# Kernel optimization log

Hardware: AMD Instinct MI355X
Metric: run time of the kernel (lower is better)

Reference implementation:

```python
import jax, jax.numpy as jnp
import numpy as np

N = 100000       # nodes
E = 1600000      # edges
V = 50000        # vocab
H = 256          # embedding dim (hsize)
A = 64           # per-head out dim (asize)
NH = 3           # num_heads
G = 64           # graphs in batch


def setup_inputs() -> dict:
    key = jax.random.key(0)
    ks = jax.random.split(key, 12)
    h0 = jax.random.randint(ks[0], (N,), 0, V)
    src = jax.random.randint(ks[1], (E,), 0, N)
    dst = jax.random.randint(ks[2], (E,), 0, N)
    graph_ids = jnp.sort(jax.random.randint(ks[3], (N,), 0, G))
    s = 0.05
    emb = jax.random.normal(ks[4], (V, H), jnp.float32) * s
    W_fc = jax.random.normal(ks[5], (H, NH * A), jnp.float32) * s   # GATConv fc
    attn_l = jax.random.normal(ks[6], (NH, A), jnp.float32) * s
    attn_r = jax.random.normal(ks[7], (NH, A), jnp.float32) * s
    bias_gat = jax.random.normal(ks[8], (NH, A), jnp.float32) * s
    W1 = jax.random.normal(ks[9], (A, 128), jnp.float32) * s
    b1 = jnp.zeros((128,), jnp.float32)
    W2 = jax.random.normal(ks[10], (128, 16), jnp.float32) * s
    b2 = jnp.zeros((16,), jnp.float32)
    return dict(h0=h0, src=src, dst=dst, graph_ids=graph_ids, emb=emb,
                W_fc=W_fc, attn_l=attn_l, attn_r=attn_r, bias_gat=bias_gat,
                W1=W1, b1=b1, W2=W2, b2=b2)


def reference(h0, src, dst, graph_ids, emb, W_fc, attn_l, attn_r, bias_gat,
              W1, b1, W2, b2):
    # embedding lookup
    h1 = emb[h0]                                            # [N, H]
    # GATConv: linear projection per head
    feat = (h1 @ W_fc).reshape(N, NH, A)                    # [N, NH, A]
    el = jnp.einsum('nha,ha->nh', feat, attn_l)             # [N, NH]
    er = jnp.einsum('nha,ha->nh', feat, attn_r)             # [N, NH]
    e = jax.nn.leaky_relu(el[src] + er[dst], 0.2)           # [E, NH]
    # segment softmax over incoming edges of each dst node
    m = jax.ops.segment_max(e, dst, num_segments=N)         # [N, NH]
    e_exp = jnp.exp(e - m[dst])                             # [E, NH]
    denom = jax.ops.segment_sum(e_exp, dst, num_segments=N) # [N, NH]
    alpha = e_exp / denom[dst]                              # [E, NH]
    # scatter-aggregate messages
    msg = alpha[:, :, None] * feat[src]                     # [E, NH, A]
    rst = jax.ops.segment_sum(msg, dst, num_segments=N)     # [N, NH, A]
    rst = rst + bias_gat[None]                              # GATConv bias
    # relu + mean over heads
    h2 = jnp.mean(jax.nn.relu(rst), axis=1)                 # [N, A]
    # MLP predictor: ReLU then Identity
    h3 = jax.nn.relu(h2 @ W1 + b1) @ W2 + b2                # [N, 16]
    # dgl.mean_nodes: per-graph mean readout
    sums = jax.ops.segment_sum(h3, graph_ids, num_segments=G)            # [G, 16]
    counts = jax.ops.segment_sum(jnp.ones((N,), h3.dtype), graph_ids, num_segments=G)
    return sums / jnp.maximum(counts, 1.0)[:, None]         # [G, 16]
```

## Files before the change

### kernel.cpp

```cpp
#include <hip/hip_runtime.h>
#include <hip/hip_bf16.h>

#define NNODES 100000
#define NEDGES 1600000
#define VOCAB 50000
#define HDIM 256
#define ADIM 64
#define NHEADS 3
#define FDIM 192
#define NGRAPH 64
#define NPART 64

typedef __attribute__((ext_vector_type(8))) short bf16x8;
typedef __attribute__((ext_vector_type(4))) float f32x4;

__device__ __forceinline__ float bf2f(unsigned short u) {
  return __uint_as_float((unsigned int)u << 16);
}
__device__ __forceinline__ unsigned short f2bf(float f) {
  unsigned int u = __float_as_uint(f);
  u += 0x7FFFu + ((u >> 16) & 1u);
  return (unsigned short)(u >> 16);
}

__global__ __launch_bounds__(256) void conv_emb_kernel(
    const float* __restrict__ emb, unsigned short* __restrict__ emb_bf, int n)
{
  int i = (blockIdx.x * 256 + threadIdx.x) * 4;
  if (i >= n) return;
  float4 v = *reinterpret_cast<const float4*>(&emb[i]);
  ushort4 o;
  o.x = f2bf(v.x); o.y = f2bf(v.y); o.z = f2bf(v.z); o.w = f2bf(v.w);
  *reinterpret_cast<ushort4*>(&emb_bf[i]) = o;
}

__global__ __launch_bounds__(256) void conv_weights_kernel(
    const float* __restrict__ Wfc, const float* __restrict__ W1,
    const float* __restrict__ W2, unsigned short* __restrict__ Wt,
    unsigned short* __restrict__ W1t, unsigned short* __restrict__ W2t)
{
  int i = blockIdx.x * 256 + threadIdx.x;
  if (i < HDIM * FDIM) {
    int c = i / HDIM, k = i % HDIM;
    Wt[i] = f2bf(Wfc[(size_t)k * FDIM + c]);
  } else if (i < HDIM * FDIM + 128 * 64) {
    int j = i - HDIM * FDIM;
    int c = j / 64, k = j % 64;
    W1t[j] = f2bf(W1[(size_t)k * 128 + c]);
  } else if (i < HDIM * FDIM + 128 * 64 + 16 * 128) {
    int j = i - HDIM * FDIM - 128 * 64;
    int c = j / 128, k = j % 128;
    W2t[j] = f2bf(W2[(size_t)k * 16 + c]);
  }
}

__global__ __launch_bounds__(256) void proj_gemm_kernel(
    const unsigned short* __restrict__ emb_bf,
    const unsigned short* __restrict__ Wt,
    unsigned short* __restrict__ proj_bf,
    int V)
{
  const int wave = threadIdx.x >> 6;
  const int lane = threadIdx.x & 63;
  const int row0 = blockIdx.x * 64 + wave * 16;
  int arow = row0 + (lane & 15);
  if (arow >= V) arow = V - 1;
  const int kgrp = (lane >> 4) * 8;

  f32x4 acc[12];
#pragma unroll
  for (int c = 0; c < 12; ++c) acc[c] = (f32x4){0.f, 0.f, 0.f, 0.f};

  const unsigned short* arow_p = &emb_bf[(size_t)arow * HDIM + kgrp];
  const unsigned short* bcol_p = &Wt[(size_t)(lane & 15) * HDIM + kgrp];

#pragma unroll
  for (int ks = 0; ks < 8; ++ks) {
    bf16x8 a = *reinterpret_cast<const bf16x8*>(arow_p + ks * 32);
#pragma unroll
    for (int c = 0; c < 12; ++c) {
      bf16x8 b = *reinterpret_cast<const bf16x8*>(bcol_p + (size_t)c * 16 * HDIM + ks * 32);
      acc[c] = __builtin_amdgcn_mfma_f32_16x16x32_bf16(a, b, acc[c], 0, 0, 0);
    }
  }
  const int cb = lane & 15;
  const int rb = row0 + 4 * (lane >> 4);
#pragma unroll
  for (int i = 0; i < 4; ++i) {
    int r = rb + i;
    if (r < V) {
#pragma unroll
      for (int c = 0; c < 12; ++c)
        proj_bf[(size_t)r * FDIM + c * 16 + cb] = f2bf(acc[c][i]);
    }
  }
}

__global__ __launch_bounds__(256) void vattn_kernel(
    const unsigned short* __restrict__ proj_bf, const float* __restrict__ attn_l,
    const float* __restrict__ attn_r, float* __restrict__ elv,
    float* __restrict__ erv, int V)
{
  int v    = blockIdx.x * 4 + (threadIdx.x >> 6);
  int lane = threadIdx.x & 63;
  if (v >= V) return;
  float sl[3], sr[3];
#pragma unroll
  for (int h = 0; h < 3; ++h) {
    float f = bf2f(proj_bf[(size_t)v * FDIM + h * 64 + lane]);
    sl[h] = f * attn_l[h * 64 + lane];
    sr[h] = f * attn_r[h * 64 + lane];
  }
#pragma unroll
  for (int s = 32; s > 0; s >>= 1) {
#pragma unroll
    for (int h = 0; h < 3; ++h) {
      sl[h] += __shfl_xor(sl[h], s, 64);
      sr[h] += __shfl_xor(sr[h], s, 64);
    }
  }
  if (lane == 0) {
#pragma unroll
    for (int h = 0; h < 3; ++h) { elv[v * 3 + h] = sl[h]; erv[v * 3 + h] = sr[h]; }
  }
}

__global__ __launch_bounds__(256) void ngather_kernel(
    const int* __restrict__ h0, const float* __restrict__ elv,
    const float* __restrict__ erv, float* __restrict__ nel,
    float* __restrict__ ner, int N)
{
  int n = blockIdx.x * 256 + threadIdx.x;
  if (n >= N) return;
  int v = h0[n];
#pragma unroll
  for (int h = 0; h < 3; ++h) {
    nel[n * 3 + h] = elv[v * 3 + h];
    ner[n * 3 + h] = erv[v * 3 + h];
  }
}

__global__ __launch_bounds__(256) void hist_kernel(
    const int* __restrict__ dst, int* __restrict__ cnt, int E)
{
  int e = blockIdx.x * 256 + threadIdx.x;
  if (e < E) atomicAdd(&cnt[dst[e]], 1);
}

__global__ __launch_bounds__(256) void scan_sum_kernel(
    const int* __restrict__ cnt, int* __restrict__ bsum, int n)
{
  __shared__ int red[256];
  int t = threadIdx.x;
  int base = blockIdx.x * 1024 + t * 4;
  int s = 0;
#pragma unroll
  for (int j = 0; j < 4; ++j) if (base + j < n) s += cnt[base + j];
  red[t] = s;
  __syncthreads();
  for (int o = 128; o > 0; o >>= 1) {
    if (t < o) red[t] += red[t + o];
    __syncthreads();
  }
  if (t == 0) bsum[blockIdx.x] = red[0];
}

__global__ void scan_bsum_kernel(int* bsum, int nb)
{
  if (threadIdx.x == 0 && blockIdx.x == 0) {
    int acc = 0;
    for (int i = 0; i < nb; ++i) { int v = bsum[i]; bsum[i] = acc; acc += v; }
  }
}

__global__ __launch_bounds__(256) void scan_write_kernel(
    const int* __restrict__ cnt, const int* __restrict__ bsum,
    int* __restrict__ offs, int n, int total)
{
  __shared__ int sd[256];
  int t = threadIdx.x;
  int base = blockIdx.x * 1024 + t * 4;
  int c[4];
  int ts = 0;
#pragma unroll
  for (int j = 0; j < 4; ++j) { c[j] = (base + j < n) ? cnt[base + j] : 0; ts += c[j]; }
  sd[t] = ts;
  __syncthreads();
  for (int o = 1; o < 256; o <<= 1) {
    int v = (t >= o) ? sd[t - o] : 0;
    __syncthreads();
    sd[t] += v;
    __syncthreads();
  }
  int run = sd[t] - ts + bsum[blockIdx.x];
#pragma unroll
  for (int j = 0; j < 4; ++j) {
    if (base + j < n) offs[base + j] = run;
    run += c[j];
  }
  if (blockIdx.x == 0 && t == 0) offs[n] = total;
}

__global__ __launch_bounds__(256) void scatter_kernel(
    const int* __restrict__ src, const int* __restrict__ dst,
    const int* __restrict__ h0,
    const float* __restrict__ nel, const float* __restrict__ ner,
    const int* __restrict__ offs, int* __restrict__ cursor,
    uint2* __restrict__ recs, int E)
{
  int e = blockIdx.x * 256 + threadIdx.x;
  if (e >= E) return;
  int s = src[e], d = dst[e];
  float w[3];
#pragma unroll
  for (int h = 0; h < 3; ++h) {
    float ev = nel[s * 3 + h] + ner[d * 3 + h];
    ev = ev > 0.f ? ev : 0.2f * ev;
    w[h] = __expf(ev);
  }
  int p = offs[d] + atomicAdd(&cursor[d], 1);
  uint2 r;
  r.x = (unsigned)h0[s] | ((unsigned)f2bf(w[0]) << 16);
  r.y = (unsigned)f2bf(w[1]) | ((unsigned)f2bf(w[2]) << 16);
  recs[p] = r;
}

__global__ __launch_bounds__(256) void aggregate_kernel(
    const uint2* __restrict__ recs, const int* __restrict__ offs,
    const unsigned short* __restrict__ proj_bf, const float* __restrict__ bias_gat,
    unsigned short* __restrict__ h2bf, int N)
{
  int lane = threadIdx.x & 63;
  int n = blockIdx.x * 4 + (threadIdx.x >> 6);
  if (n >= N) return;
  int lo = offs[n], hi = offs[n + 1];
  float a0 = 0.f, a1 = 0.f, a2 = 0.f, d0 = 0.f, d1 = 0.f, d2 = 0.f;

  int i = lo;
  for (; i + 4 <= hi; i += 4) {
    uint2 r[4];
#pragma unroll
    for (int j = 0; j < 4; ++j) r[j] = recs[i + j];
    const unsigned short* ps[4];
#pragma unroll
    for (int j = 0; j < 4; ++j)
      ps[j] = &proj_bf[(size_t)(r[j].x & 0xFFFFu) * FDIM];
    float g0[4], g1[4], g2[4];
#pragma unroll
    for (int j = 0; j < 4; ++j) {
      g0[j] = bf2f(ps[j][lane]);
      g1[j] = bf2f(ps[j][64 + lane]);
      g2[j] = bf2f(ps[j][128 + lane]);
    }
#pragma unroll
    for (int j = 0; j < 4; ++j) {
      float w0 = bf2f((unsigned short)(r[j].x >> 16));
      float w1 = bf2f((unsigned short)(r[j].y & 0xFFFFu));
      float w2 = bf2f((unsigned short)(r[j].y >> 16));
      a0 += w0 * g0[j]; a1 += w1 * g1[j]; a2 += w2 * g2[j];
      d0 += w0; d1 += w1; d2 += w2;
    }
  }
  for (; i < hi; ++i) {
    uint2 r = recs[i];
    const unsigned short* ps = &proj_bf[(size_t)(r.x & 0xFFFFu) * FDIM];
    float w0 = bf2f((unsigned short)(r.x >> 16));
    float w1 = bf2f((unsigned short)(r.y & 0xFFFFu));
    float w2 = bf2f((unsigned short)(r.y >> 16));
    a0 += w0 * bf2f(ps[lane]);
    a1 += w1 * bf2f(ps[64 + lane]);
    a2 += w2 * bf2f(ps[128 + lane]);
    d0 += w0; d1 += w1; d2 += w2;
  }

  float i0 = d0 > 0.f ? 1.f / d0 : 0.f;
  float i1 = d1 > 0.f ? 1.f / d1 : 0.f;
  float i2 = d2 > 0.f ? 1.f / d2 : 0.f;
  float r0 = a0 * i0 + bias_gat[lane];
  float r1 = a1 * i1 + bias_gat[64 + lane];
  float r2 = a2 * i2 + bias_gat[128 + lane];
  float h2 = (fmaxf(r0, 0.f) + fmaxf(r1, 0.f) + fmaxf(r2, 0.f)) * (1.f / 3.f);
  h2bf[(size_t)n * 64 + lane] = f2bf(h2);
}

__global__ __launch_bounds__(256) void post_mfma_kernel(
    const unsigned short* __restrict__ h2bf,
    const unsigned short* __restrict__ W1t,
    const float* __restrict__ b1,
    const unsigned short* __restrict__ W2t,
    const float* __restrict__ b2, const int* __restrict__ gid,
    float* __restrict__ sums_priv, float* __restrict__ counts_priv, int N)
{
  __shared__ unsigned short z_lds[64 * 128];
  const int wave = threadIdx.x >> 6;
  const int lane = threadIdx.x & 63;
  const int r = lane & 15;
  const int q = lane >> 4;
  const int kg = q * 8;
  const int rw0 = blockIdx.x * 64 + wave * 16;

  int arow = rw0 + r;
  if (arow >= N) arow = N - 1;

  f32x4 acc1[8];
#pragma unroll
  for (int c = 0; c < 8; ++c) acc1[c] = (f32x4){0.f, 0.f, 0.f, 0.f};

#pragma unroll
  for (int ks = 0; ks < 2; ++ks) {
    bf16x8 a = *reinterpret_cast<const bf16x8*>(&h2bf[(size_t)arow * 64 + kg + ks * 32]);
#pragma unroll
    for (int c = 0; c < 8; ++c) {
      bf16x8 b = *reinterpret_cast<const bf16x8*>(&W1t[(size_t)(c * 16 + r) * 64 + kg + ks * 32]);
      acc1[c] = __builtin_amdgcn_mfma_f32_16x16x32_bf16(a, b, acc1[c], 0, 0, 0);
    }
  }
#pragma unroll
  for (int c = 0; c < 8; ++c) {
    float bb = b1[c * 16 + r];
#pragma unroll
    for (int i = 0; i < 4; ++i) {
      float z = acc1[c][i] + bb;
      z = z > 0.f ? z : 0.f;
      z_lds[(wave * 16 + 4 * q + i) * 128 + c * 16 + r] = f2bf(z);
    }
  }
  __syncthreads();

  f32x4 acc2 = (f32x4){0.f, 0.f, 0.f, 0.f};
#pragma unroll
  for (int ks = 0; ks < 4; ++ks) {
    bf16x8 a = *reinterpret_cast<const bf16x8*>(&z_lds[(wave * 16 + r) * 128 + kg + ks * 32]);
    bf16x8 b = *reinterpret_cast<const bf16x8*>(&W2t[(size_t)r * 128 + kg + ks * 32]);
    acc2 = __builtin_amdgcn_mfma_f32_16x16x32_bf16(a, b, acc2, 0, 0, 0);
  }
  const int part = blockIdx.x & (NPART - 1);
  float bb2 = b2[r];
#pragma unroll
  for (int i = 0; i < 4; ++i) {
    int row = rw0 + 4 * q + i;
    if (row < N) {
      int g = gid[row];
      atomicAdd(&sums_priv[(part * NGRAPH + g) * 16 + r], acc2[i] + bb2);
      if (r == 0) atomicAdd(&counts_priv[part * NGRAPH + g], 1.f);
    }
  }
}

__global__ void finalize_kernel(const float* __restrict__ sums_priv,
                                const float* __restrict__ counts_priv,
                                float* __restrict__ out)
{
  int j = threadIdx.x;
  int g = j >> 4;
  float s = 0.f, c = 0.f;
  for (int p = 0; p < NPART; ++p) {
    s += sums_priv[p * NGRAPH * 16 + j];
    c += counts_priv[p * NGRAPH + g];
  }
  out[j] = s / fmaxf(c, 1.f);
}

extern "C" void kernel_launch(void* const* d_in, const int* in_sizes, int n_in,
                              void* d_out, int out_size, void* d_ws, size_t ws_size,
                              hipStream_t stream)
{
  const int*   h0  = (const int*)  d_in[0];
  const int*   src = (const int*)  d_in[1];
  const int*   dst = (const int*)  d_in[2];
  const int*   gid = (const int*)  d_in[3];
  const float* emb = (const float*)d_in[4];
  const float* Wfc = (const float*)d_in[5];
  const float* al  = (const float*)d_in[6];
  const float* ar  = (const float*)d_in[7];
  const float* bg  = (const float*)d_in[8];
  const float* W1  = (const float*)d_in[9];
  const float* b1  = (const float*)d_in[10];
  const float* W2  = (const float*)d_in[11];
  const float* b2  = (const float*)d_in[12];
  float* out = (float*)d_out;

  char* ws = (char*)d_ws;
  size_t off = 0;
  auto alloc = [&](size_t bytes) -> void* {
    off = (off + 255) & ~(size_t)255;
    void* p = ws + off;
    off += bytes;
    return p;
  };
  unsigned short* emb_bf  = (unsigned short*)alloc((size_t)VOCAB * HDIM * 2);
  unsigned short* Wt      = (unsigned short*)alloc((size_t)FDIM * HDIM * 2);
  unsigned short* W1t     = (unsigned short*)alloc((size_t)128 * 64 * 2);
  unsigned short* W2t     = (unsigned short*)alloc((size_t)16 * 128 * 2);
  unsigned short* proj_bf = (unsigned short*)alloc((size_t)VOCAB * FDIM * 2);
  unsigned short* h2bf    = (unsigned short*)alloc((size_t)NNODES * 64 * 2);
  uint2*  recs   = (uint2*) alloc((size_t)NEDGES * 8);
  float*  elv    = (float*) alloc((size_t)VOCAB * 3 * 4);
  float*  erv    = (float*) alloc((size_t)VOCAB * 3 * 4);
  float*  nel    = (float*) alloc((size_t)NNODES * 3 * 4);
  float*  ner    = (float*) alloc((size_t)NNODES * 3 * 4);
  int*    cnt    = (int*)   alloc((size_t)NNODES * 4);
  int*    offs   = (int*)   alloc((size_t)(NNODES + 1) * 4);
  int*    cursor = (int*)   alloc((size_t)NNODES * 4);
  int*    bsum   = (int*)   alloc((size_t)128 * 4);
  float*  sums   = (float*) alloc((size_t)NPART * NGRAPH * 16 * 4);
  float*  cnts   = (float*) alloc((size_t)NPART * NGRAPH * 4);

  hipMemsetAsync(cnt,    0, (size_t)NNODES * 4, stream);
  hipMemsetAsync(cursor, 0, (size_t)NNODES * 4, stream);
  hipMemsetAsync(sums,   0, (size_t)NPART * NGRAPH * 16 * 4, stream);
  hipMemsetAsync(cnts,   0, (size_t)NPART * NGRAPH * 4, stream);

  const int NB = (NNODES + 1023) / 1024;

  conv_emb_kernel<<<(VOCAB * HDIM / 4 + 255) / 256, 256, 0, stream>>>(
      emb, emb_bf, VOCAB * HDIM);
  conv_weights_kernel<<<(HDIM * FDIM + 128 * 64 + 16 * 128 + 255) / 256, 256, 0, stream>>>(
      Wfc, W1, W2, Wt, W1t, W2t);
  proj_gemm_kernel<<<(VOCAB + 63) / 64, 256, 0, stream>>>(emb_bf, Wt, proj_bf, VOCAB);
  vattn_kernel<<<(VOCAB + 3) / 4, 256, 0, stream>>>(proj_bf, al, ar, elv, erv, VOCAB);
  ngather_kernel<<<(NNODES + 255) / 256, 256, 0, stream>>>(h0, elv, erv, nel, ner, NNODES);
  hist_kernel<<<(NEDGES + 255) / 256, 256, 0, stream>>>(dst, cnt, NEDGES);
  scan_sum_kernel<<<NB, 256, 0, stream>>>(cnt, bsum, NNODES);
  scan_bsum_kernel<<<1, 64, 0, stream>>>(bsum, NB);
  scan_write_kernel<<<NB, 256, 0, stream>>>(cnt, bsum, offs, NNODES, NEDGES);
  scatter_kernel<<<(NEDGES + 255) / 256, 256, 0, stream>>>(src, dst, h0, nel, ner, offs,
                                                           cursor, recs, NEDGES);
  aggregate_kernel<<<(NNODES + 3) / 4, 256, 0, stream>>>(recs, offs, proj_bf, bg,
                                                         h2bf, NNODES);
  post_mfma_kernel<<<(NNODES + 63) / 64, 256, 0, stream>>>(h2bf, W1t, b1, W2t, b2, gid,
                                                           sums, cnts, NNODES);
  finalize_kernel<<<1, 1024, 0, stream>>>(sums, cnts, out);
}
```

Before: 393.2 us.

## Fuse emb conversion and attention scores into projection GEMM, shrink edge records

Folds the fp32-to-bf16 embedding conversion and the per-vocab attention dot products into the projection GEMM epilogue, removing the conv_emb, vattn and ngather kernels. The histogram kernel now records each edge's atomic rank, so scatter needs no second atomic cursor pass. Edge records shrink from 8-byte packed weights to a 16-bit vocab index, and attention weights are recomputed in the aggregate kernel from float4 el/er tables. This cuts launches and edge-array traffic but adds exp work and an extra gather per edge during aggregation. It also assumes per-node in-degree fits in 16 bits.

```diff
diff --git a/kernel.cpp b/kernel.cpp
--- a/kernel.cpp
+++ b/kernel.cpp
@@ -21,17 +21,6 @@
   unsigned int u = __float_as_uint(f);
   u += 0x7FFFu + ((u >> 16) & 1u);
   return (unsigned short)(u >> 16);
-}
-
-__global__ __launch_bounds__(256) void conv_emb_kernel(
-    const float* __restrict__ emb, unsigned short* __restrict__ emb_bf, int n)
-{
-  int i = (blockIdx.x * 256 + threadIdx.x) * 4;
-  if (i >= n) return;
-  float4 v = *reinterpret_cast<const float4*>(&emb[i]);
-  ushort4 o;
-  o.x = f2bf(v.x); o.y = f2bf(v.y); o.z = f2bf(v.z); o.w = f2bf(v.w);
-  *reinterpret_cast<ushort4*>(&emb_bf[i]) = o;
 }
 
 __global__ __launch_bounds__(256) void conv_weights_kernel(
@@ -55,36 +44,46 @@
 }
 
 __global__ __launch_bounds__(256) void proj_gemm_kernel(
-    const unsigned short* __restrict__ emb_bf,
+    const float* __restrict__ emb,
     const unsigned short* __restrict__ Wt,
+    const float* __restrict__ attn_l,
+    const float* __restrict__ attn_r,
     unsigned short* __restrict__ proj_bf,
-    int V)
+    float4* __restrict__ elv4, float4* __restrict__ erv4, int V)
 {
   const int wave = threadIdx.x >> 6;
   const int lane = threadIdx.x & 63;
   const int row0 = blockIdx.x * 64 + wave * 16;
-  int arow = row0 + (lane & 15);
+  const int cb = lane & 15;
+  const int q  = lane >> 4;
+  int arow = row0 + cb;
   if (arow >= V) arow = V - 1;
-  const int kgrp = (lane >> 4) * 8;
+  const int kgrp = q * 8;
 
   f32x4 acc[12];
 #pragma unroll
   for (int c = 0; c < 12; ++c) acc[c] = (f32x4){0.f, 0.f, 0.f, 0.f};
 
-  const unsigned short* arow_p = &emb_bf[(size_t)arow * HDIM + kgrp];
-  const unsigned short* bcol_p = &Wt[(size_t)(lane & 15) * HDIM + kgrp];
+  const float* arow_p = &emb[(size_t)arow * HDIM + kgrp];
+  const unsigned short* bcol_p = &Wt[(size_t)cb * HDIM + kgrp];
 
 #pragma unroll
   for (int ks = 0; ks < 8; ++ks) {
-    bf16x8 a = *reinterpret_cast<const bf16x8*>(arow_p + ks * 32);
+    float4 f0 = *reinterpret_cast<const float4*>(arow_p + ks * 32);
+    float4 f1 = *reinterpret_cast<const float4*>(arow_p + ks * 32 + 4);
+    bf16x8 a;
+    a[0] = (short)f2bf(f0.x); a[1] = (short)f2bf(f0.y);
+    a[2] = (short)f2bf(f0.z); a[3] = (short)f2bf(f0.w);
+    a[4] = (short)f2bf(f1.x); a[5] = (short)f2bf(f1.y);
+    a[6] = (short)f2bf(f1.z); a[7] = (short)f2bf(f1.w);
 #pragma unroll
     for (int c = 0; c < 12; ++c) {
       bf16x8 b = *reinterpret_cast<const bf16x8*>(bcol_p + (size_t)c * 16 * HDIM + ks * 32);
       acc[c] = __builtin_amdgcn_mfma_f32_16x16x32_bf16(a, b, acc[c], 0, 0, 0);
     }
   }
-  const int cb = lane & 15;
-  const int rb = row0 + 4 * (lane >> 4);
+
+  const int rb = row0 + 4 * q;
 #pragma unroll
   for (int i = 0; i < 4; ++i) {
     int r = rb + i;
@@ -94,57 +93,55 @@
         proj_bf[(size_t)r * FDIM + c * 16 + cb] = f2bf(acc[c][i]);
     }
   }
-}
-
-__global__ __launch_bounds__(256) void vattn_kernel(
-    const unsigned short* __restrict__ proj_bf, const float* __restrict__ attn_l,
-    const float* __restrict__ attn_r, float* __restrict__ elv,
-    float* __restrict__ erv, int V)
-{
-  int v    = blockIdx.x * 4 + (threadIdx.x >> 6);
-  int lane = threadIdx.x & 63;
-  if (v >= V) return;
-  float sl[3], sr[3];
-#pragma unroll
-  for (int h = 0; h < 3; ++h) {
-    float f = bf2f(proj_bf[(size_t)v * FDIM + h * 64 + lane]);
-    sl[h] = f * attn_l[h * 64 + lane];
-    sr[h] = f * attn_r[h * 64 + lane];
-  }
-#pragma unroll
-  for (int s = 32; s > 0; s >>= 1) {
+
+  float al_v[12], ar_v[12];
+#pragma unroll
+  for (int c = 0; c < 12; ++c) {
+    al_v[c] = attn_l[c * 16 + cb];
+    ar_v[c] = attn_r[c * 16 + cb];
+  }
+  float elp[4][3], erp[4][3];
+#pragma unroll
+  for (int i = 0; i < 4; ++i)
 #pragma unroll
     for (int h = 0; h < 3; ++h) {
-      sl[h] += __shfl_xor(sl[h], s, 64);
-      sr[h] += __shfl_xor(sr[h], s, 64);
-    }
-  }
-  if (lane == 0) {
-#pragma unroll
-    for (int h = 0; h < 3; ++h) { elv[v * 3 + h] = sl[h]; erv[v * 3 + h] = sr[h]; }
-  }
-}
-
-__global__ __launch_bounds__(256) void ngather_kernel(
-    const int* __restrict__ h0, const float* __restrict__ elv,
-    const float* __restrict__ erv, float* __restrict__ nel,
-    float* __restrict__ ner, int N)
-{
-  int n = blockIdx.x * 256 + threadIdx.x;
-  if (n >= N) return;
-  int v = h0[n];
-#pragma unroll
-  for (int h = 0; h < 3; ++h) {
-    nel[n * 3 + h] = elv[v * 3 + h];
-    ner[n * 3 + h] = erv[v * 3 + h];
+      float sl = 0.f, sr = 0.f;
+#pragma unroll
+      for (int cc = 0; cc < 4; ++cc) {
+        float v = acc[h * 4 + cc][i];
+        sl += v * al_v[h * 4 + cc];
+        sr += v * ar_v[h * 4 + cc];
+      }
+      elp[i][h] = sl; erp[i][h] = sr;
+    }
+#pragma unroll
+  for (int s = 8; s > 0; s >>= 1) {
+#pragma unroll
+    for (int i = 0; i < 4; ++i)
+#pragma unroll
+      for (int h = 0; h < 3; ++h) {
+        elp[i][h] += __shfl_xor(elp[i][h], s, 64);
+        erp[i][h] += __shfl_xor(erp[i][h], s, 64);
+      }
+  }
+  if (cb == 0) {
+#pragma unroll
+    for (int i = 0; i < 4; ++i) {
+      int r = rb + i;
+      if (r < V) {
+        elv4[r] = make_float4(elp[i][0], elp[i][1], elp[i][2], 0.f);
+        erv4[r] = make_float4(erp[i][0], erp[i][1], erp[i][2], 0.f);
+      }
+    }
   }
 }
 
 __global__ __launch_bounds__(256) void hist_kernel(
-    const int* __restrict__ dst, int* __restrict__ cnt, int E)
+    const int* __restrict__ dst, int* __restrict__ cnt,
+    unsigned short* __restrict__ rank16, int E)
 {
   int e = blockIdx.x * 256 + threadIdx.x;
-  if (e < E) atomicAdd(&cnt[dst[e]], 1);
+  if (e < E) rank16[e] = (unsigned short)atomicAdd(&cnt[dst[e]], 1);
 }
 
 __global__ __launch_bounds__(256) void scan_sum_kernel(
@@ -203,48 +200,41 @@
 
 __global__ __launch_bounds__(256) void scatter_kernel(
     const int* __restrict__ src, const int* __restrict__ dst,
-    const int* __restrict__ h0,
-    const float* __restrict__ nel, const float* __restrict__ ner,
-    const int* __restrict__ offs, int* __restrict__ cursor,
-    uint2* __restrict__ recs, int E)
+    const int* __restrict__ h0, const unsigned short* __restrict__ rank16,
+    const int* __restrict__ offs, unsigned short* __restrict__ recs16, int E)
 {
   int e = blockIdx.x * 256 + threadIdx.x;
   if (e >= E) return;
-  int s = src[e], d = dst[e];
-  float w[3];
-#pragma unroll
-  for (int h = 0; h < 3; ++h) {
-    float ev = nel[s * 3 + h] + ner[d * 3 + h];
-    ev = ev > 0.f ? ev : 0.2f * ev;
-    w[h] = __expf(ev);
-  }
-  int p = offs[d] + atomicAdd(&cursor[d], 1);
-  uint2 r;
-  r.x = (unsigned)h0[s] | ((unsigned)f2bf(w[0]) << 16);
-  r.y = (unsigned)f2bf(w[1]) | ((unsigned)f2bf(w[2]) << 16);
-  recs[p] = r;
+  int p = offs[dst[e]] + (int)rank16[e];
+  recs16[p] = (unsigned short)h0[src[e]];
 }
 
 __global__ __launch_bounds__(256) void aggregate_kernel(
-    const uint2* __restrict__ recs, const int* __restrict__ offs,
-    const unsigned short* __restrict__ proj_bf, const float* __restrict__ bias_gat,
+    const unsigned short* __restrict__ recs16, const int* __restrict__ offs,
+    const int* __restrict__ h0,
+    const unsigned short* __restrict__ proj_bf,
+    const float4* __restrict__ elv4, const float4* __restrict__ erv4,
+    const float* __restrict__ bias_gat,
     unsigned short* __restrict__ h2bf, int N)
 {
   int lane = threadIdx.x & 63;
   int n = blockIdx.x * 4 + (threadIdx.x >> 6);
   if (n >= N) return;
+  const float4 ero = erv4[h0[n]];
   int lo = offs[n], hi = offs[n + 1];
   float a0 = 0.f, a1 = 0.f, a2 = 0.f, d0 = 0.f, d1 = 0.f, d2 = 0.f;
 
   int i = lo;
   for (; i + 4 <= hi; i += 4) {
-    uint2 r[4];
-#pragma unroll
-    for (int j = 0; j < 4; ++j) r[j] = recs[i + j];
+    int vs[4];
+#pragma unroll
+    for (int j = 0; j < 4; ++j) vs[j] = recs16[i + j];
+    float4 ev[4];
+#pragma unroll
+    for (int j = 0; j < 4; ++j) ev[j] = elv4[vs[j]];
     const unsigned short* ps[4];
 #pragma unroll
-    for (int j = 0; j < 4; ++j)
-      ps[j] = &proj_bf[(size_t)(r[j].x & 0xFFFFu) * FDIM];
+    for (int j = 0; j < 4; ++j) ps[j] = &proj_bf[(size_t)vs[j] * FDIM];
     float g0[4], g1[4], g2[4];
 #pragma unroll
     for (int j = 0; j < 4; ++j) {
@@ -254,19 +244,24 @@
     }
 #pragma unroll
     for (int j = 0; j < 4; ++j) {
-      float w0 = bf2f((unsigned short)(r[j].x >> 16));
-      float w1 = bf2f((unsigned short)(r[j].y & 0xFFFFu));
-      float w2 = bf2f((unsigned short)(r[j].y >> 16));
+      float e0 = ev[j].x + ero.x, e1 = ev[j].y + ero.y, e2 = ev[j].z + ero.z;
+      e0 = e0 > 0.f ? e0 : 0.2f * e0;
+      e1 = e1 > 0.f ? e1 : 0.2f * e1;
+      e2 = e2 > 0.f ? e2 : 0.2f * e2;
+      float w0 = __expf(e0), w1 = __expf(e1), w2 = __expf(e2);
       a0 += w0 * g0[j]; a1 += w1 * g1[j]; a2 += w2 * g2[j];
       d0 += w0; d1 += w1; d2 += w2;
     }
   }
   for (; i < hi; ++i) {
-    uint2 r = recs[i];
-    const unsigned short* ps = &proj_bf[(size_t)(r.x & 0xFFFFu) * FDIM];
-    float w0 = bf2f((unsigned short)(r.x >> 16));
-    float w1 = bf2f((unsigned short)(r.y & 0xFFFFu));
-    float w2 = bf2f((unsigned short)(r.y >> 16));
+    int vs = recs16[i];
+    float4 ev = elv4[vs];
+    const unsigned short* ps = &proj_bf[(size_t)vs * FDIM];
+    float e0 = ev.x + ero.x, e1 = ev.y + ero.y, e2 = ev.z + ero.z;
+    e0 = e0 > 0.f ? e0 : 0.2f * e0;
+    e1 = e1 > 0.f ? e1 : 0.2f * e1;
+    e2 = e2 > 0.f ? e2 : 0.2f * e2;
+    float w0 = __expf(e0), w1 = __expf(e1), w2 = __expf(e2);
     a0 += w0 * bf2f(ps[lane]);
     a1 += w1 * bf2f(ps[64 + lane]);
     a2 += w2 * bf2f(ps[128 + lane]);
@@ -388,46 +383,39 @@
     off += bytes;
     return p;
   };
-  unsigned short* emb_bf  = (unsigned short*)alloc((size_t)VOCAB * HDIM * 2);
   unsigned short* Wt      = (unsigned short*)alloc((size_t)FDIM * HDIM * 2);
   unsigned short* W1t     = (unsigned short*)alloc((size_t)128 * 64 * 2);
   unsigned short* W2t     = (unsigned short*)alloc((size_t)16 * 128 * 2);
   unsigned short* proj_bf = (unsigned short*)alloc((size_t)VOCAB * FDIM * 2);
   unsigned short* h2bf    = (unsigned short*)alloc((size_t)NNODES * 64 * 2);
-  uint2*  recs   = (uint2*) alloc((size_t)NEDGES * 8);
-  float*  elv    = (float*) alloc((size_t)VOCAB * 3 * 4);
-  float*  erv    = (float*) alloc((size_t)VOCAB * 3 * 4);
-  float*  nel    = (float*) alloc((size_t)NNODES * 3 * 4);
-  float*  ner    = (float*) alloc((size_t)NNODES * 3 * 4);
+  unsigned short* recs16  = (unsigned short*)alloc((size_t)NEDGES * 2);
+  unsigned short* rank16  = (unsigned short*)alloc((size_t)NEDGES * 2);
+  float4* elv4   = (float4*)alloc((size_t)VOCAB * 16);
+  float4* erv4   = (float4*)alloc((size_t)VOCAB * 16);
   int*    cnt    = (int*)   alloc((size_t)NNODES * 4);
   int*    offs   = (int*)   alloc((size_t)(NNODES + 1) * 4);
-  int*    cursor = (int*)   alloc((size_t)NNODES * 4);
   int*    bsum   = (int*)   alloc((size_t)128 * 4);
   float*  sums   = (float*) alloc((size_t)NPART * NGRAPH * 16 * 4);
   float*  cnts   = (float*) alloc((size_t)NPART * NGRAPH * 4);
 
-  hipMemsetAsync(cnt,    0, (size_t)NNODES * 4, stream);
-  hipMemsetAsync(cursor, 0, (size_t)NNODES * 4, stream);
-  hipMemsetAsync(sums,   0, (size_t)NPART * NGRAPH * 16 * 4, stream);
-  hipMemsetAsync(cnts,   0, (size_t)NPART * NGRAPH * 4, stream);
+  hipMemsetAsync(cnt,  0, (size_t)NNODES * 4, stream);
+  hipMemsetAsync(sums, 0, (size_t)NPART * NGRAPH * 16 * 4, stream);
+  hipMemsetAsync(cnts, 0, (size_t)NPART * NGRAPH * 4, stream);
 
   const int NB = (NNODES + 1023) / 1024;
 
-  conv_emb_kernel<<<(VOCAB * HDIM / 4 + 255) / 256, 256, 0, stream>>>(
-      emb, emb_bf, VOCAB * HDIM);
   conv_weights_kernel<<<(HDIM * FDIM + 128 * 64 + 16 * 128 + 255) / 256, 256, 0, stream>>>(
       Wfc, W1, W2, Wt, W1t, W2t);
-  proj_gemm_kernel<<<(VOCAB + 63) / 64, 256, 0, stream>>>(emb_bf, Wt, proj_bf, VOCAB);
-  vattn_kernel<<<(VOCAB + 3) / 4, 256, 0, stream>>>(proj_bf, al, ar, elv, erv, VOCAB);
-  ngather_kernel<<<(NNODES + 255) / 256, 256, 0, stream>>>(h0, elv, erv, nel, ner, NNODES);
-  hist_kernel<<<(NEDGES + 255) / 256, 256, 0, stream>>>(dst, cnt, NEDGES);
+  proj_gemm_kernel<<<(VOCAB + 63) / 64, 256, 0, stream>>>(emb, Wt, al, ar,
+                                                          proj_bf, elv4, erv4, VOCAB);
+  hist_kernel<<<(NEDGES + 255) / 256, 256, 0, stream>>>(dst, cnt, rank16, NEDGES);
   scan_sum_kernel<<<NB, 256, 0, stream>>>(cnt, bsum, NNODES);
   scan_bsum_kernel<<<1, 64, 0, stream>>>(bsum, NB);
   scan_write_kernel<<<NB, 256, 0, stream>>>(cnt, bsum, offs, NNODES, NEDGES);
-  scatter_kernel<<<(NEDGES + 255) / 256, 256, 0, stream>>>(src, dst, h0, nel, ner, offs,
-                                                           cursor, recs, NEDGES);
-  aggregate_kernel<<<(NNODES + 3) / 4, 256, 0, stream>>>(recs, offs, proj_bf, bg,
-                                                         h2bf, NNODES);
+  scatter_kernel<<<(NEDGES + 255) / 256, 256, 0, stream>>>(src, dst, h0, rank16, offs,
+                                                           recs16, NEDGES);
+  aggregate_kernel<<<(NNODES + 3) / 4, 256, 0, stream>>>(recs16, offs, h0, proj_bf,
+                                                         elv4, erv4, bg, h2bf, NNODES);
   post_mfma_kernel<<<(NNODES + 63) / 64, 256, 0, stream>>>(h2bf, W1t, b1, W2t, b2, gid,
                                                            sums, cnts, NNODES);
   finalize_kernel<<<1, 1024, 0, stream>>>(sums, cnts, out);
```

New measurement: 356.9 us. 1.1x faster.
